# Kernel tuning notes

Measured on AMD Instinct MI355X. Metric: run time of the kernel, lower is better.

The kernel has to match this reference:

```python
import jax, jax.numpy as jnp
import numpy as np

B, S, DIM, RANK = 2, 1024, 256, 32


def setup_inputs() -> dict:
    key = jax.random.key(0)
    k_x, k_A, k_W = jax.random.split(key, 3)
    x = jax.random.normal(k_x, (B, S, DIM), dtype=jnp.float32)
    A = jax.random.normal(k_A, (RANK, DIM), dtype=jnp.float32) * 0.02
    log_lambda = jnp.log(jnp.asarray(0.1, dtype=jnp.float32))
    # position_mod Linear(dim, rank): W [rank, dim], b [rank]
    bound = 1.0 / np.sqrt(DIM)
    W = jax.random.uniform(k_W, (RANK, DIM), minval=-bound, maxval=bound, dtype=jnp.float32)
    b = jnp.zeros((RANK,), dtype=jnp.float32)
    return {"x": x, "A": A, "log_lambda": log_lambda, "W": W, "b": b}


def reference(x, A, log_lambda, W, b):
    # mod = tanh(Linear(x)): [b, s, rank]
    mod = jnp.tanh(jnp.einsum('bsd,rd->bsr', x, W) + b)
    # A_mod[b,s,r,i] = A[r,i] * mod[b,s,r]
    A_mod = mod[..., None] * A  # [b, s, rank, dim]
    # g = sum_r A_mod[...,r,i] * A_mod[...,r,j] : position-modulated low-rank Gram
    g = jnp.einsum('bsri,bsrj->bsij', A_mod, A_mod)  # [b, s, dim, dim]
    lam = jnp.exp(log_lambda)
    eye = jnp.eye(A.shape[1], dtype=g.dtype)
    return g + lam * eye
```

## Files before the change

### kernel.cpp

```cpp
#include <hip/hip_runtime.h>
#include <math.h>


constexpr int DIM  = 256;
constexpr int RANK = 32;
constexpr int AT_STRIDE = RANK + 4;

typedef float f32x4 __attribute__((ext_vector_type(4)));

__global__ __launch_bounds__(256, 2) void riemannian_metric_kernel(
    const float* __restrict__ x,
    const float* __restrict__ A,
    const float* __restrict__ log_lambda,
    const float* __restrict__ W,
    const float* __restrict__ bvec,
    float* __restrict__ out)
{
    __shared__ float xs[DIM];
    __shared__ float sw[RANK];
    __shared__ float at[DIM * AT_STRIDE];

    const int tid = threadIdx.x;
    const int pos = blockIdx.x;
    const int cg  = tid & 63;
    const int rs  = tid >> 6;
    const int j0  = cg * 4;

    f32x4 aj[RANK];
    #pragma unroll
    for (int r = 0; r < RANK; ++r)
        aj[r] = *(const f32x4*)(A + r * DIM + j0);

    xs[tid] = x[(size_t)pos * DIM + tid];
    #pragma unroll
    for (int r = 0; r < RANK; ++r)
        at[tid * AT_STRIDE + r] = A[r * DIM + tid];
    __syncthreads();

    {
        const int r = tid >> 3, seg = tid & 7;
        const f32x4* wr4 = (const f32x4*)(W + r * DIM + seg * 32);
        const f32x4* xr4 = (const f32x4*)(xs + seg * 32);
        float dot = 0.f;
        #pragma unroll
        for (int q = 0; q < 8; ++q) {
            f32x4 wv = wr4[q], xv = xr4[q];
            dot = fmaf(wv.x, xv.x, dot);
            dot = fmaf(wv.y, xv.y, dot);
            dot = fmaf(wv.z, xv.z, dot);
            dot = fmaf(wv.w, xv.w, dot);
        }
        dot += __shfl_xor(dot, 1);
        dot += __shfl_xor(dot, 2);
        dot += __shfl_xor(dot, 4);
        if (seg == 0) {
            float m = tanhf(dot + bvec[r]);
            sw[r] = m * m;
        }
    }
    __syncthreads();

    #pragma unroll
    for (int r = 0; r < RANK; ++r) {
        float wv = sw[r];
        aj[r] *= wv;
    }

    const float lam = expf(log_lambda[0]);
    f32x4* op = (f32x4*)(out + (size_t)pos * DIM * DIM + (size_t)(rs * 64) * DIM + j0);

    #pragma unroll 2
    for (int k = 0; k < 64; ++k) {
        const int i = rs * 64 + k;
        const f32x4* row = (const f32x4*)(at + i * AT_STRIDE);
        f32x4 acc = (f32x4)(0.f);
        #pragma unroll
        for (int q = 0; q < 8; ++q) {
            f32x4 ar = row[q];
            acc += ar.x * aj[4*q+0];
            acc += ar.y * aj[4*q+1];
            acc += ar.z * aj[4*q+2];
            acc += ar.w * aj[4*q+3];
        }
        if ((i >> 2) == cg) {
            acc[i & 3] += lam;
        }
        __builtin_nontemporal_store(acc, op + (size_t)k * (DIM / 4));
    }
}

extern "C" void kernel_launch(void* const* d_in, const int* in_sizes, int n_in,
                              void* d_out, int out_size, void* d_ws, size_t ws_size,
                              hipStream_t stream) {
    const float* x          = (const float*)d_in[0];
    const float* A          = (const float*)d_in[1];
    const float* log_lambda = (const float*)d_in[2];
    const float* W          = (const float*)d_in[3];
    const float* bvec       = (const float*)d_in[4];
    float* out              = (float*)d_out;

    const int n_pos = in_sizes[0] / DIM;
    riemannian_metric_kernel<<<n_pos, 256, 0, stream>>>(x, A, log_lambda, W, bvec, out);
}
```

Before: 135.5 us.

## Broadcast A rows via readlane instead of LDS transpose buffer

Drops the padded shared-memory transpose of A. Each output row's A coefficients are fetched from the register-resident scaled A columns with cross-lane readlane. Each side is scaled by |tanh| instead of scaling one side by tanh², which keeps the Gram product unchanged. This removes about 36KB of LDS per block and the per-block transpose loads, aiming at higher occupancy and less setup. The cost is many scalar readlane operations inside the inner loop.

```diff
diff --git a/kernel.cpp b/kernel.cpp
--- a/kernel.cpp
+++ b/kernel.cpp
@@ -4,9 +4,13 @@
 
 constexpr int DIM  = 256;
 constexpr int RANK = 32;
-constexpr int AT_STRIDE = RANK + 4;
 
 typedef float f32x4 __attribute__((ext_vector_type(4)));
+
+static __device__ __forceinline__ float readlane_f32(float v, int lane) {
+    return __builtin_bit_cast(float,
+        __builtin_amdgcn_readlane(__builtin_bit_cast(int, v), lane));
+}
 
 __global__ __launch_bounds__(256, 2) void riemannian_metric_kernel(
     const float* __restrict__ x,
@@ -18,7 +22,6 @@
 {
     __shared__ float xs[DIM];
     __shared__ float sw[RANK];
-    __shared__ float at[DIM * AT_STRIDE];
 
     const int tid = threadIdx.x;
     const int pos = blockIdx.x;
@@ -32,9 +35,6 @@
         aj[r] = *(const f32x4*)(A + r * DIM + j0);
 
     xs[tid] = x[(size_t)pos * DIM + tid];
-    #pragma unroll
-    for (int r = 0; r < RANK; ++r)
-        at[tid * AT_STRIDE + r] = A[r * DIM + tid];
     __syncthreads();
 
     {
@@ -53,39 +53,32 @@
         dot += __shfl_xor(dot, 1);
         dot += __shfl_xor(dot, 2);
         dot += __shfl_xor(dot, 4);
-        if (seg == 0) {
-            float m = tanhf(dot + bvec[r]);
-            sw[r] = m * m;
-        }
+        if (seg == 0) sw[r] = fabsf(tanhf(dot + bvec[r]));
     }
     __syncthreads();
 
     #pragma unroll
-    for (int r = 0; r < RANK; ++r) {
-        float wv = sw[r];
-        aj[r] *= wv;
-    }
+    for (int r = 0; r < RANK; ++r)
+        aj[r] *= sw[r];
 
     const float lam = expf(log_lambda[0]);
     f32x4* op = (f32x4*)(out + (size_t)pos * DIM * DIM + (size_t)(rs * 64) * DIM + j0);
 
-    #pragma unroll 2
-    for (int k = 0; k < 64; ++k) {
-        const int i = rs * 64 + k;
-        const f32x4* row = (const f32x4*)(at + i * AT_STRIDE);
-        f32x4 acc = (f32x4)(0.f);
+    #pragma unroll 1
+    for (int kb = 0; kb < 16; ++kb) {
+        const int lane = rs * 16 + kb;
         #pragma unroll
-        for (int q = 0; q < 8; ++q) {
-            f32x4 ar = row[q];
-            acc += ar.x * aj[4*q+0];
-            acc += ar.y * aj[4*q+1];
-            acc += ar.z * aj[4*q+2];
-            acc += ar.w * aj[4*q+3];
+        for (int c = 0; c < 4; ++c) {
+            f32x4 acc = (f32x4)(0.f);
+            #pragma unroll
+            for (int r = 0; r < RANK; ++r) {
+                float s = readlane_f32(aj[r][c], lane);
+                acc += s * aj[r];
+            }
+            const int i = rs * 64 + kb * 4 + c;
+            if ((i >> 2) == cg) acc[i & 3] += lam;
+            __builtin_nontemporal_store(acc, op + (size_t)(kb * 4 + c) * (DIM / 4));
         }
-        if ((i >> 2) == cg) {
-            acc[i & 3] += lam;
-        }
-        __builtin_nontemporal_store(acc, op + (size_t)k * (DIM / 4));
     }
 }
 
```

Measured after the change: 146.3 us. +8.0%, slower.
